# Kernel tuning notes

Measured on AMD Instinct MI355X. Metric: run time of the kernel, lower is better.

Reference implementation:

```python
import jax, jax.numpy as jnp
import numpy as np

TAU = 0.2  # temperature from __init__
EPS = 1e-12  # F.normalize eps


def setup_inputs() -> dict:
    key = jax.random.key(0)
    k1, k2, k3 = jax.random.split(key, 3)
    N, D = 131072, 1024
    return {
        "query": jax.random.normal(k1, (D,), dtype=jnp.float32),
        "K": jax.random.normal(k2, (N, D), dtype=jnp.float32),
        "V": jax.random.normal(k3, (N, D), dtype=jnp.float32),
        "topk": 32,
    }


def reference(query, K, V, topk):
    # q = F.normalize(query, dim=-1)
    q = query / jnp.maximum(jnp.linalg.norm(query, axis=-1, keepdims=True), EPS)
    # logits: [N] cosine-sim / tau (K rows are assumed pre-normalized by write())
    logits = (K @ q) / TAU
    # top-k branch (N > topk)
    vals, idxs = jax.lax.top_k(logits, topk)          # [topk], [topk]
    attn = jax.nn.softmax(vals, axis=-1)              # [topk]
    out = attn @ V[idxs]                              # [D]
    full_attn = jnp.zeros_like(logits).at[idxs].set(attn)  # [N]
    return out, full_attn
```

## Files before the change

kernel.cpp:

```cpp
#include <hip/hip_runtime.h>
#include <float.h>
#include <math.h>

#define DIM   1024
#define NROWS 131072
#define TOPK  32
#define TAU   0.2f

__global__ __launch_bounds__(256) void norm_kernel(const float* __restrict__ q,
                                                   float* __restrict__ scale_out) {
    __shared__ float red[4];
    int t = threadIdx.x;
    float ss = 0.f;
    for (int i = t; i < DIM; i += 256) { float v = q[i]; ss += v * v; }
    #pragma unroll
    for (int off = 32; off > 0; off >>= 1) ss += __shfl_xor(ss, off, 64);
    int wave = t >> 6;
    if ((t & 63) == 0) red[wave] = ss;
    __syncthreads();
    if (t == 0) {
        float s = red[0] + red[1] + red[2] + red[3];
        float nrm = fmaxf(sqrtf(s), 1e-12f);
        scale_out[0] = 1.0f / (nrm * TAU);
    }
}

__global__ __launch_bounds__(256) void logits_kernel(const float* __restrict__ Km,
                                                     const float* __restrict__ q,
                                                     const float* __restrict__ scale_p,
                                                     float* __restrict__ logits,
                                                     float* __restrict__ full_attn) {
    const int lane = threadIdx.x & 63;
    const int wave = threadIdx.x >> 6;
    const int gwave = blockIdx.x * 4 + wave;
    const int total_waves = gridDim.x * 4;
    const float scale = scale_p[0];

    float4 qv[4];
    #pragma unroll
    for (int c = 0; c < 4; ++c)
        qv[c] = *reinterpret_cast<const float4*>(q + c * 256 + lane * 4);

    for (int row = gwave; row < NROWS; row += total_waves) {
        const float* kr = Km + (size_t)row * DIM;
        float acc = 0.f;
        #pragma unroll
        for (int c = 0; c < 4; ++c) {
            float4 kv = *reinterpret_cast<const float4*>(kr + c * 256 + lane * 4);
            acc += qv[c].x * kv.x + qv[c].y * kv.y + qv[c].z * kv.z + qv[c].w * kv.w;
        }
        #pragma unroll
        for (int off = 32; off > 0; off >>= 1) acc += __shfl_xor(acc, off, 64);
        if (lane == 0) {
            logits[row] = acc * scale;
            full_attn[row] = 0.0f;
        }
    }
}

__global__ __launch_bounds__(64) void topk_local_kernel(const float* __restrict__ logits,
                                                        float* __restrict__ cand_val,
                                                        int* __restrict__ cand_idx) {
    const int lane = threadIdx.x;
    const int base = blockIdx.x * 512;

    float v[8]; int gi[8];
    float4 a = *reinterpret_cast<const float4*>(logits + base + lane * 4);
    float4 b = *reinterpret_cast<const float4*>(logits + base + 256 + lane * 4);
    v[0] = a.x; v[1] = a.y; v[2] = a.z; v[3] = a.w;
    v[4] = b.x; v[5] = b.y; v[6] = b.z; v[7] = b.w;
    #pragma unroll
    for (int j = 0; j < 4; ++j) gi[j] = base + lane * 4 + j;
    #pragma unroll
    for (int j = 0; j < 4; ++j) gi[4 + j] = base + 256 + lane * 4 + j;

    for (int r = 0; r < TOPK; ++r) {
        float m = v[0]; int mi = gi[0];
        #pragma unroll
        for (int j = 1; j < 8; ++j)
            if (v[j] > m || (v[j] == m && gi[j] < mi)) { m = v[j]; mi = gi[j]; }
        #pragma unroll
        for (int off = 32; off > 0; off >>= 1) {
            float ov = __shfl_xor(m, off, 64);
            int   oi = __shfl_xor(mi, off, 64);
            if (ov > m || (ov == m && oi < mi)) { m = ov; mi = oi; }
        }
        #pragma unroll
        for (int j = 0; j < 8; ++j)
            if (gi[j] == mi) v[j] = -FLT_MAX;
        if (lane == 0) {
            cand_val[blockIdx.x * TOPK + r] = m;
            cand_idx[blockIdx.x * TOPK + r] = mi;
        }
    }
}

__global__ __launch_bounds__(256) void final_kernel(const float* __restrict__ cand_val,
                                                    const int* __restrict__ cand_idx,
                                                    const float* __restrict__ Vm,
                                                    float* __restrict__ out,
                                                    float* __restrict__ full_attn) {
    const int t = threadIdx.x;
    const int lane = t & 63, wave = t >> 6;
    __shared__ float wred_v[4];
    __shared__ int   wred_i[4];
    __shared__ float tval[TOPK];
    __shared__ int   tidx[TOPK];
    __shared__ float attn_s[TOPK];

    float v[32]; int gi[32];
    #pragma unroll
    for (int k = 0; k < 32; ++k) {
        int c = t + 256 * k;
        v[k]  = cand_val[c];
        gi[k] = cand_idx[c];
    }

    for (int r = 0; r < TOPK; ++r) {
        float m = v[0]; int mi = gi[0];
        #pragma unroll
        for (int k = 1; k < 32; ++k)
            if (v[k] > m || (v[k] == m && gi[k] < mi)) { m = v[k]; mi = gi[k]; }
        #pragma unroll
        for (int off = 32; off > 0; off >>= 1) {
            float ov = __shfl_xor(m, off, 64);
            int   oi = __shfl_xor(mi, off, 64);
            if (ov > m || (ov == m && oi < mi)) { m = ov; mi = oi; }
        }
        if (lane == 0) { wred_v[wave] = m; wred_i[wave] = mi; }
        __syncthreads();
        m = wred_v[0]; mi = wred_i[0];
        #pragma unroll
        for (int w = 1; w < 4; ++w) {
            float ov = wred_v[w]; int oi = wred_i[w];
            if (ov > m || (ov == m && oi < mi)) { m = ov; mi = oi; }
        }
        #pragma unroll
        for (int k = 0; k < 32; ++k)
            if (gi[k] == mi) v[k] = -FLT_MAX;
        if (t == 0) { tval[r] = m; tidx[r] = mi; }
        __syncthreads();
    }

    float mx = tval[0];
    float sum = 0.f;
    #pragma unroll
    for (int j = 0; j < TOPK; ++j) sum += expf(tval[j] - mx);
    if (t < TOPK) attn_s[t] = expf(tval[t] - mx) / sum;
    __syncthreads();

    if (t < TOPK) full_attn[tidx[t]] = attn_s[t];

    for (int d = t; d < DIM; d += 256) {
        float acc = 0.f;
        #pragma unroll
        for (int j = 0; j < TOPK; ++j)
            acc += attn_s[j] * Vm[(size_t)tidx[j] * DIM + d];
        out[d] = acc;
    }
}

extern "C" void kernel_launch(void* const* d_in, const int* in_sizes, int n_in,
                              void* d_out, int out_size, void* d_ws, size_t ws_size,
                              hipStream_t stream) {
    const float* q  = (const float*)d_in[0];
    const float* Km = (const float*)d_in[1];
    const float* Vm = (const float*)d_in[2];

    float* out       = (float*)d_out;
    float* full_attn = out + DIM;

    char*  ws       = (char*)d_ws;
    float* scale    = (float*)ws;
    float* logits   = (float*)(ws + 256);
    float* cand_val = logits + NROWS;
    int*   cand_idx = (int*)(cand_val + 8192);

    norm_kernel<<<1, 256, 0, stream>>>(q, scale);
    logits_kernel<<<8192, 256, 0, stream>>>(Km, q, scale, logits, full_attn);
    topk_local_kernel<<<NROWS / 512, 64, 0, stream>>>(logits, cand_val, cand_idx);
    final_kernel<<<1, 256, 0, stream>>>(cand_val, cand_idx, Vm, out, full_attn);
}
```

Baseline: 201.8 us.

## Defer query scaling to softmax, drop norm kernel, restructure logits and final top-k

```diff
diff --git a/kernel.cpp b/kernel.cpp
--- a/kernel.cpp
+++ b/kernel.cpp
@@ -2,59 +2,48 @@
 #include <float.h>
 #include <math.h>
 
-#define DIM   1024
-#define NROWS 131072
-#define TOPK  32
-#define TAU   0.2f
-
-__global__ __launch_bounds__(256) void norm_kernel(const float* __restrict__ q,
-                                                   float* __restrict__ scale_out) {
-    __shared__ float red[4];
-    int t = threadIdx.x;
-    float ss = 0.f;
-    for (int i = t; i < DIM; i += 256) { float v = q[i]; ss += v * v; }
-    #pragma unroll
-    for (int off = 32; off > 0; off >>= 1) ss += __shfl_xor(ss, off, 64);
-    int wave = t >> 6;
-    if ((t & 63) == 0) red[wave] = ss;
-    __syncthreads();
-    if (t == 0) {
-        float s = red[0] + red[1] + red[2] + red[3];
-        float nrm = fmaxf(sqrtf(s), 1e-12f);
-        scale_out[0] = 1.0f / (nrm * TAU);
-    }
-}
+#define DIM    1024
+#define NROWS  131072
+#define TOPK   32
+#define TAU    0.2f
+#define CHUNK  512
+#define NCHUNK (NROWS / CHUNK)
+#define NCAND  (NCHUNK * TOPK)
 
 __global__ __launch_bounds__(256) void logits_kernel(const float* __restrict__ Km,
                                                      const float* __restrict__ q,
-                                                     const float* __restrict__ scale_p,
                                                      float* __restrict__ logits,
                                                      float* __restrict__ full_attn) {
-    const int lane = threadIdx.x & 63;
-    const int wave = threadIdx.x >> 6;
-    const int gwave = blockIdx.x * 4 + wave;
-    const int total_waves = gridDim.x * 4;
-    const float scale = scale_p[0];
+    __shared__ float q_s[DIM];
+    const int t = threadIdx.x;
+    *reinterpret_cast<float4*>(q_s + t * 4) =
+        *reinterpret_cast<const float4*>(q + t * 4);
+    __syncthreads();
 
-    float4 qv[4];
+    const int lane = t & 63;
+    const int wave = t >> 6;
+    const int sub  = lane & 15;
+    const int rsel = lane >> 4;
+    const int row  = (blockIdx.x * 4 + wave) * 4 + rsel;
+
+    const float* kr = Km + (size_t)row * DIM;
+    float acc = 0.f;
     #pragma unroll
-    for (int c = 0; c < 4; ++c)
-        qv[c] = *reinterpret_cast<const float4*>(q + c * 256 + lane * 4);
+    for (int c = 0; c < 16; ++c) {
+        const int fo = c * 64 + sub * 4;
+        float4 kv = *reinterpret_cast<const float4*>(kr + fo);
+        float4 qv = *reinterpret_cast<const float4*>(q_s + fo);
+        acc = fmaf(kv.x, qv.x, acc);
+        acc = fmaf(kv.y, qv.y, acc);
+        acc = fmaf(kv.z, qv.z, acc);
+        acc = fmaf(kv.w, qv.w, acc);
+    }
+    #pragma unroll
+    for (int off = 1; off < 16; off <<= 1) acc += __shfl_xor(acc, off, 64);
 
-    for (int row = gwave; row < NROWS; row += total_waves) {
-        const float* kr = Km + (size_t)row * DIM;
-        float acc = 0.f;
-        #pragma unroll
-        for (int c = 0; c < 4; ++c) {
-            float4 kv = *reinterpret_cast<const float4*>(kr + c * 256 + lane * 4);
-            acc += qv[c].x * kv.x + qv[c].y * kv.y + qv[c].z * kv.z + qv[c].w * kv.w;
-        }
-        #pragma unroll
-        for (int off = 32; off > 0; off >>= 1) acc += __shfl_xor(acc, off, 64);
-        if (lane == 0) {
-            logits[row] = acc * scale;
-            full_attn[row] = 0.0f;
-        }
+    if (sub == 0) {
+        logits[row]    = acc;
+        full_attn[row] = 0.f;
     }
 }
 
@@ -62,7 +51,7 @@
                                                         float* __restrict__ cand_val,
                                                         int* __restrict__ cand_idx) {
     const int lane = threadIdx.x;
-    const int base = blockIdx.x * 512;
+    const int base = blockIdx.x * CHUNK;
 
     float v[8]; int gi[8];
     float4 a = *reinterpret_cast<const float4*>(logits + base + lane * 4);
@@ -97,6 +86,7 @@
 
 __global__ __launch_bounds__(256) void final_kernel(const float* __restrict__ cand_val,
                                                     const int* __restrict__ cand_idx,
+                                                    const float* __restrict__ q,
                                                     const float* __restrict__ Vm,
                                                     float* __restrict__ out,
                                                     float* __restrict__ full_attn) {
@@ -107,6 +97,19 @@
     __shared__ float tval[TOPK];
     __shared__ int   tidx[TOPK];
     __shared__ float attn_s[TOPK];
+    __shared__ float red4[4];
+    __shared__ float scale_s;
+
+    float ss = 0.f;
+    for (int i = t; i < DIM; i += 256) { float vq = q[i]; ss = fmaf(vq, vq, ss); }
+    #pragma unroll
+    for (int off = 32; off > 0; off >>= 1) ss += __shfl_xor(ss, off, 64);
+    if (lane == 0) red4[wave] = ss;
+    __syncthreads();
+    if (t == 0) {
+        float s = red4[0] + red4[1] + red4[2] + red4[3];
+        scale_s = 1.0f / (fmaxf(sqrtf(s), 1e-12f) * TAU);
+    }
 
     float v[32]; int gi[32];
     #pragma unroll
@@ -115,38 +118,47 @@
         v[k]  = cand_val[c];
         gi[k] = cand_idx[c];
     }
+    float m = v[0]; int mi = gi[0];
+    #pragma unroll
+    for (int k = 1; k < 32; ++k)
+        if (v[k] > m || (v[k] == m && gi[k] < mi)) { m = v[k]; mi = gi[k]; }
+
+    __syncthreads();
 
     for (int r = 0; r < TOPK; ++r) {
-        float m = v[0]; int mi = gi[0];
-        #pragma unroll
-        for (int k = 1; k < 32; ++k)
-            if (v[k] > m || (v[k] == m && gi[k] < mi)) { m = v[k]; mi = gi[k]; }
+        float wm = m; int wmi = mi;
         #pragma unroll
         for (int off = 32; off > 0; off >>= 1) {
-            float ov = __shfl_xor(m, off, 64);
-            int   oi = __shfl_xor(mi, off, 64);
-            if (ov > m || (ov == m && oi < mi)) { m = ov; mi = oi; }
+            float ov = __shfl_xor(wm, off, 64);
+            int   oi = __shfl_xor(wmi, off, 64);
+            if (ov > wm || (ov == wm && oi < wmi)) { wm = ov; wmi = oi; }
         }
-        if (lane == 0) { wred_v[wave] = m; wred_i[wave] = mi; }
+        if (lane == 0) { wred_v[wave] = wm; wred_i[wave] = wmi; }
         __syncthreads();
-        m = wred_v[0]; mi = wred_i[0];
+        float gm = wred_v[0]; int gmi = wred_i[0];
         #pragma unroll
         for (int w = 1; w < 4; ++w) {
             float ov = wred_v[w]; int oi = wred_i[w];
-            if (ov > m || (ov == m && oi < mi)) { m = ov; mi = oi; }
+            if (ov > gm || (ov == gm && oi < gmi)) { gm = ov; gmi = oi; }
         }
-        #pragma unroll
-        for (int k = 0; k < 32; ++k)
-            if (gi[k] == mi) v[k] = -FLT_MAX;
-        if (t == 0) { tval[r] = m; tidx[r] = mi; }
+        if (t == 0) { tval[r] = gm; tidx[r] = gmi; }
+        if (mi == gmi) {
+            #pragma unroll
+            for (int k = 0; k < 32; ++k)
+                if (gi[k] == gmi) v[k] = -FLT_MAX;
+            m = v[0]; mi = gi[0];
+            #pragma unroll
+            for (int k = 1; k < 32; ++k)
+                if (v[k] > m || (v[k] == m && gi[k] < mi)) { m = v[k]; mi = gi[k]; }
+        }
         __syncthreads();
     }
 
-    float mx = tval[0];
+    const float scale = scale_s;
     float sum = 0.f;
     #pragma unroll
-    for (int j = 0; j < TOPK; ++j) sum += expf(tval[j] - mx);
-    if (t < TOPK) attn_s[t] = expf(tval[t] - mx) / sum;
+    for (int j = 0; j < TOPK; ++j) sum += expf((tval[j] - tval[0]) * scale);
+    if (t < TOPK) attn_s[t] = expf((tval[t] - tval[0]) * scale) / sum;
     __syncthreads();
 
     if (t < TOPK) full_attn[tidx[t]] = attn_s[t];
@@ -155,7 +167,7 @@
         float acc = 0.f;
         #pragma unroll
         for (int j = 0; j < TOPK; ++j)
-            acc += attn_s[j] * Vm[(size_t)tidx[j] * DIM + d];
+            acc = fmaf(attn_s[j], Vm[(size_t)tidx[j] * DIM + d], acc);
         out[d] = acc;
     }
 }
@@ -170,14 +182,11 @@
     float* out       = (float*)d_out;
     float* full_attn = out + DIM;
 
-    char*  ws       = (char*)d_ws;
-    float* scale    = (float*)ws;
-    float* logits   = (float*)(ws + 256);
+    float* logits   = (float*)d_ws;
     float* cand_val = logits + NROWS;
-    int*   cand_idx = (int*)(cand_val + 8192);
+    int*   cand_idx = (int*)(cand_val + NCAND);
 
-    norm_kernel<<<1, 256, 0, stream>>>(q, scale);
-    logits_kernel<<<8192, 256, 0, stream>>>(Km, q, scale, logits, full_attn);
-    topk_local_kernel<<<NROWS / 512, 64, 0, stream>>>(logits, cand_val, cand_idx);
-    final_kernel<<<1, 256, 0, stream>>>(cand_val, cand_idx, Vm, out, full_attn);
+    logits_kernel<<<NROWS / 16, 256, 0, stream>>>(Km, q, logits, full_attn);
+    topk_local_kernel<<<NCHUNK, 64, 0, stream>>>(logits, cand_val, cand_idx);
+    final_kernel<<<1, 256, 0, stream>>>(cand_val, cand_idx, q, Vm, out, full_attn);
 }
```

New measurement: 202.2 us. No clear change (+0.2%).
